# Kernel optimization log

Measured on AMD Instinct MI355X. Metric: run time of the kernel, lower is better.

Reference implementation:

```python
import jax, jax.numpy as jnp
import numpy as np

B, N, C, H, K = 4, 16384, 256, 8, 64
D = C // H
EPS = 1e-8

def setup_inputs() -> dict:
    key = jax.random.key(0)
    ks = jax.random.split(key, 6)
    scale = 0.02
    return {
        "voxel_features": jax.random.normal(ks[0], (B, N, C), dtype=jnp.float32),
        "cluster_assignments": jax.random.uniform(ks[1], (B, N, K), dtype=jnp.float32),
        "w_qkv": jax.random.normal(ks[2], (C, 3 * C), dtype=jnp.float32) * scale,
        "w_proj": jax.random.normal(ks[3], (C, C), dtype=jnp.float32) * scale,
        "b_proj": jnp.zeros((C,), dtype=jnp.float32),
        "cluster_bias": jax.random.normal(ks[4], (K, K), dtype=jnp.float32) * scale,
    }

def reference(voxel_features, cluster_assignments, w_qkv, w_proj, b_proj, cluster_bias):
    b, n, c = voxel_features.shape
    h, d = H, c // H
    A = cluster_assignments                                  # (B,N,K)
    qkv = (voxel_features @ w_qkv).reshape(b, n, 3, h, d)    # (B,N,3,H,D)
    q = jnp.moveaxis(qkv[:, :, 0], 1, 2)                     # (B,H,N,D)
    k = jnp.moveaxis(qkv[:, :, 1], 1, 2)
    v = jnp.moveaxis(qkv[:, :, 2], 1, 2)
    # cluster mass per (batch, cluster)
    denom = A.sum(axis=1) + EPS                              # (B,K)
    # cluster-pooled K/V: contraction over N (the huge broadcast-sum in torch)
    k_cluster = jnp.einsum('bnk,bhnd->bhkd', A, k) / denom[:, None, :, None]
    v_cluster = jnp.einsum('bnk,bhnd->bhkd', A, v) / denom[:, None, :, None]
    attn = jnp.einsum('bhnd,bhkd->bhnk', q, k_cluster) * (d ** -0.5)
    bias = jnp.einsum('bnk,kl->bnl', A, cluster_bias)        # (B,N,K)
    attn = jax.nn.softmax(attn + bias[:, None, :, :], axis=-1)
    x = jnp.einsum('bhnk,bhkd->bhnd', attn, v_cluster)       # (B,H,N,D)
    x = jnp.moveaxis(x, 1, 2).reshape(b, n, c)               # (B,N,C)
    return x @ w_proj + b_proj
```

## Files before the change

### kernel.cpp

```cpp
#include <hip/hip_runtime.h>

#define NTOK 16384
#define BATCH 4

typedef __attribute__((ext_vector_type(8))) short bf16x8;
typedef __attribute__((ext_vector_type(8))) unsigned short ushort8;
typedef __attribute__((ext_vector_type(4))) float f32x4;

__device__ __forceinline__ unsigned short f2bf(float f) {
  union { float f; unsigned int u; } c; c.f = f;
  unsigned int r = c.u + 0x7fff + ((c.u >> 16) & 1);
  return (unsigned short)(r >> 16);
}

__global__ __launch_bounds__(256) void zero_f(float* __restrict__ p, int n) {
  int i = blockIdx.x * 256 + threadIdx.x;
  if (i < n) p[i] = 0.f;
}

__global__ __launch_bounds__(256) void convx2(const float* __restrict__ voxel,
                                              const float* __restrict__ A,
                                              unsigned short* __restrict__ xb,
                                              unsigned short* __restrict__ Ab) {
  for (int i = blockIdx.x * 256 + threadIdx.x; i < 2621440; i += gridDim.x * 256) {
    const float* src; unsigned short* dst; int j;
    if (i < 2097152) { j = i; src = voxel; dst = xb; }
    else { j = i - 2097152; src = A; dst = Ab; }
    float4 a = *(const float4*)(src + 8 * (size_t)j);
    float4 b = *(const float4*)(src + 8 * (size_t)j + 4);
    ushort8 o;
    o[0] = f2bf(a.x); o[1] = f2bf(a.y); o[2] = f2bf(a.z); o[3] = f2bf(a.w);
    o[4] = f2bf(b.x); o[5] = f2bf(b.y); o[6] = f2bf(b.z); o[7] = f2bf(b.w);
    *(ushort8*)(dst + 8 * (size_t)j) = o;
  }
}

__global__ __launch_bounds__(256) void convw(const float* __restrict__ w_qkv,
                                             const float* __restrict__ w_proj,
                                             const float* __restrict__ cb,
                                             unsigned short* __restrict__ wqT,
                                             unsigned short* __restrict__ wpT,
                                             unsigned short* __restrict__ cbbT) {
  int n = blockIdx.x, k = threadIdx.x;
  if (n < 256) wqT[n * 256 + k] = f2bf(w_qkv[(size_t)k * 768 + n]);
  else if (n < 512) wpT[(n - 256) * 256 + k] = f2bf(w_proj[(size_t)k * 256 + (n - 256)]);
  else if (n == 512 && k < 64) {
    for (int j = 0; j < 64; ++j) cbbT[k * 64 + j] = f2bf(cb[j * 64 + k]);
  }
}

template <int ADD_BIAS, int C_BF16>
__global__ __launch_bounds__(256, 3) void gemm_mfma(const unsigned short* __restrict__ Ab,
                                                    const unsigned short* __restrict__ BT,
                                                    const float* __restrict__ bias,
                                                    void* __restrict__ Cv,
                                                    int N, int K, int lda) {
  __shared__ __align__(16) unsigned short smem[2][128][72];
  const int tid = threadIdx.x;
  int bx, by;
  if ((gridDim.y & 7) == 0) {
    int flat = blockIdx.y * gridDim.x + blockIdx.x;
    int xc = flat & 7, t = flat >> 3;
    int gx = gridDim.x, ypx = gridDim.y >> 3;
    bx = t % gx; by = xc * ypx + t / gx;
  } else { bx = blockIdx.x; by = blockIdx.y; }
  const int bn = bx * 128, bm = by * 128;
  const int lane = tid & 63;
  const int wv = tid >> 6;
  const int wm = wv & 1, wn = wv >> 1;
  const int m16 = lane & 15, quad = lane >> 4;

  const int srow = tid >> 1;
  const int scol = (tid & 1) * 32;

  const unsigned short* ga = Ab + (size_t)(bm + srow) * lda + scol;
  const unsigned short* gb = BT + (size_t)(bn + srow) * K + scol;

  ushort8 ra[2][4], rb[2][4];
#pragma unroll
  for (int kt = 0; kt < 2; ++kt)
#pragma unroll
    for (int i = 0; i < 4; ++i) {
      ra[kt][i] = *(const ushort8*)(ga + kt * 64 + 8 * i);
      rb[kt][i] = *(const ushort8*)(gb + kt * 64 + 8 * i);
    }

  f32x4 acc[4][4];
#pragma unroll
  for (int r = 0; r < 4; ++r)
#pragma unroll
    for (int c = 0; c < 4; ++c) acc[r][c] = (f32x4){0.f, 0.f, 0.f, 0.f};

#pragma unroll
  for (int kt = 0; kt < 4; ++kt) {
    const int sb = kt & 1;
    if (kt > 0) __syncthreads();
#pragma unroll
    for (int i = 0; i < 4; ++i) {
      *(ushort8*)&smem[0][srow][scol + 8 * i] = ra[sb][i];
      *(ushort8*)&smem[1][srow][scol + 8 * i] = rb[sb][i];
    }
    __syncthreads();
    if (kt < 2) {
#pragma unroll
      for (int i = 0; i < 4; ++i) {
        ra[sb][i] = *(const ushort8*)(ga + (kt + 2) * 64 + 8 * i);
        rb[sb][i] = *(const ushort8*)(gb + (kt + 2) * 64 + 8 * i);
      }
    }
#pragma unroll
    for (int ks = 0; ks < 64; ks += 32) {
      bf16x8 af[4], bf[4];
#pragma unroll
      for (int r = 0; r < 4; ++r)
        af[r] = *(const bf16x8*)&smem[0][wm * 64 + r * 16 + m16][ks + quad * 8];
#pragma unroll
      for (int c = 0; c < 4; ++c)
        bf[c] = *(const bf16x8*)&smem[1][wn * 64 + c * 16 + m16][ks + quad * 8];
#pragma unroll
      for (int r = 0; r < 4; ++r)
#pragma unroll
        for (int c = 0; c < 4; ++c)
          acc[r][c] = __builtin_amdgcn_mfma_f32_16x16x32_bf16(af[r], bf[c], acc[r][c], 0, 0, 0);
    }
  }

  float bv[4];
  if (ADD_BIAS) {
#pragma unroll
    for (int c = 0; c < 4; ++c) bv[c] = bias[bn + wn * 64 + c * 16 + m16];
  }
  const int lrD = tid >> 2, cch = (tid & 3) * 32;
  unsigned short* Csh = (unsigned short*)smem;
  float* Csf = (float*)smem;
#pragma unroll
  for (int p = 0; p < 2; ++p) {
    __syncthreads();
    if (wm == p) {
#pragma unroll
      for (int r = 0; r < 4; ++r) {
        int lr0 = r * 16 + quad * 4;
#pragma unroll
        for (int c = 0; c < 4; ++c) {
          int col = wn * 64 + c * 16 + m16;
#pragma unroll
          for (int i = 0; i < 4; ++i) {
            float v = acc[r][c][i] + (ADD_BIAS ? bv[c] : 0.f);
            if (C_BF16) Csh[(lr0 + i) * 136 + col] = f2bf(v);
            else Csf[(lr0 + i) * 132 + col] = v;
          }
        }
      }
    }
    __syncthreads();
    if (C_BF16) {
      unsigned short* gp = (unsigned short*)Cv + (size_t)(bm + p * 64 + lrD) * N + bn + cch;
      const unsigned short* sp = Csh + lrD * 136 + cch;
      ushort8 t0 = *(const ushort8*)(sp + 0);
      ushort8 t1 = *(const ushort8*)(sp + 8);
      ushort8 t2 = *(const ushort8*)(sp + 16);
      ushort8 t3 = *(const ushort8*)(sp + 24);
      *(ushort8*)(gp + 0) = t0;
      *(ushort8*)(gp + 8) = t1;
      *(ushort8*)(gp + 16) = t2;
      *(ushort8*)(gp + 24) = t3;
    } else {
      float* gp = (float*)Cv + (size_t)(bm + p * 64 + lrD) * N + bn + cch;
      const float* sp = Csf + lrD * 132 + cch;
      float4 t[8];
#pragma unroll
      for (int u = 0; u < 8; ++u) t[u] = *(const float4*)(sp + 4 * u);
#pragma unroll
      for (int u = 0; u < 8; ++u) *(float4*)(gp + 4 * u) = t[u];
    }
  }
}

__global__ __launch_bounds__(256) void pool_mfma(const unsigned short* __restrict__ Ab,
                                                 const unsigned short* __restrict__ xb,
                                                 float* __restrict__ part) {
  __shared__ unsigned short At[64][40];
  __shared__ unsigned short Xt[128][40];
  const int tid = threadIdx.x;
  const int tch = blockIdx.x, cblk = blockIdx.y, b = blockIdx.z;
  const int w = tid >> 6, lane = tid & 63;
  const int m16 = lane & 15, quad = lane >> 4;
  const size_t row0 = (size_t)b * NTOK + (size_t)tch * 256;
  const int cb0 = cblk * 128;
  const int tokL = tid & 31, gA = tid >> 5;

  f32x4 acc[4][2];
#pragma unroll
  for (int r = 0; r < 4; ++r)
#pragma unroll
    for (int c = 0; c < 2; ++c) acc[r][c] = (f32x4){0.f, 0.f, 0.f, 0.f};

  ushort8 px[2], pa;
  auto loadG = [&](int t0) {
#pragma unroll
    for (int u = 0; u < 2; ++u) {
      int idx = tid + u * 256;
      int tok = idx & 31, g = idx >> 5;
      px[u] = *(const ushort8*)(xb + (row0 + t0 + tok) * 256 + cb0 + g * 8);
    }
    pa = *(const ushort8*)(Ab + (row0 + t0 + tokL) * 64 + gA * 8);
  };
  loadG(0);

  for (int ks = 0; ks < 8; ++ks) {
    __syncthreads();
#pragma unroll
    for (int u = 0; u < 2; ++u) {
      int idx = tid + u * 256;
      int tok = idx & 31, g = idx >> 5;
#pragma unroll
      for (int i = 0; i < 8; ++i) Xt[g * 8 + i][tok] = (unsigned short)px[u][i];
    }
#pragma unroll
    for (int i = 0; i < 8; ++i) At[gA * 8 + i][tokL] = (unsigned short)pa[i];
    __syncthreads();
    if (ks + 1 < 8) loadG((ks + 1) * 32);
    bf16x8 af[4], bfr[2];
#pragma unroll
    for (int r = 0; r < 4; ++r) af[r] = *(const bf16x8*)&At[r * 16 + m16][quad * 8];
#pragma unroll
    for (int c = 0; c < 2; ++c) bfr[c] = *(const bf16x8*)&Xt[w * 32 + c * 16 + m16][quad * 8];
#pragma unroll
    for (int r = 0; r < 4; ++r)
#pragma unroll
      for (int c = 0; c < 2; ++c)
        acc[r][c] = __builtin_amdgcn_mfma_f32_16x16x32_bf16(af[r], bfr[c], acc[r][c], 0, 0, 0);
  }

  float* pp = part + ((size_t)(b * 64 + tch) * 64) * 256 + cb0;
#pragma unroll
  for (int r = 0; r < 4; ++r)
#pragma unroll
    for (int c = 0; c < 2; ++c)
#pragma unroll
      for (int i = 0; i < 4; ++i) {
        int cl = r * 16 + quad * 4 + i;
        int ch = w * 32 + c * 16 + m16;
        pp[(size_t)cl * 256 + ch] = acc[r][c][i];
      }
}

__global__ __launch_bounds__(256) void pool2(const float* __restrict__ part,
                                             const float* __restrict__ asum,
                                             float* __restrict__ pooledX) {
  int id = blockIdx.x * 256 + threadIdx.x;
  int c = id & 255, cl = (id >> 8) & 63, b = id >> 14;
  const float* pp = part + ((size_t)(b * 64) * 64 + cl) * 256 + c;
  float s = 0.f;
#pragma unroll 4
  for (int t = 0; t < 64; ++t) s += pp[(size_t)t * 16384];
  float denom = asum[b * 64 + cl] + 1e-8f;
  pooledX[(size_t)(b * 64 + cl) * 256 + c] = s / denom;
}

__global__ __launch_bounds__(256) void kvgemm(const float* __restrict__ pooledX,
                                              const float* __restrict__ w_qkv,
                                              unsigned short* __restrict__ kcb,
                                              unsigned short* __restrict__ vcbT) {
  __shared__ float px[256];
  const int bc = blockIdx.x;
  const int b = bc >> 6, cl = bc & 63;
  const int tid = threadIdx.x;
  px[tid] = pooledX[(size_t)bc * 256 + tid];
  __syncthreads();
  float accK = 0.f, accV = 0.f;
#pragma unroll 8
  for (int k = 0; k < 256; ++k) {
    float x = px[k];
    accK = fmaf(x, w_qkv[(size_t)k * 768 + 256 + tid], accK);
    accV = fmaf(x, w_qkv[(size_t)k * 768 + 512 + tid], accV);
  }
  int h = tid >> 5, d = tid & 31;
  kcb[(((size_t)b * 8 + h) * 64 + cl) * 32 + d] = f2bf(accK * 0.17677669529663687f);
  vcbT[(((size_t)b * 8 + h) * 32 + d) * 64 + cl] = f2bf(accV);
}

__global__ __launch_bounds__(256) void asum_kernel(const float* __restrict__ A,
                                                   float* __restrict__ asum) {
  __shared__ float red[4][64];
  const int ch = blockIdx.x, b = blockIdx.y;
  const int jq = threadIdx.x >> 6, k = threadIdx.x & 63;
  const size_t row0 = (size_t)b * NTOK + (size_t)ch * 256;
  const float* ap = A + (row0 + jq) * 64 + k;
  float s = 0.f;
#pragma unroll 4
  for (int j = 0; j < 64; ++j) s += ap[(size_t)j * 256];
  red[jq][k] = s;
  __syncthreads();
  if (threadIdx.x < 64) {
    float v = red[0][k] + red[1][k] + red[2][k] + red[3][k];
    atomicAdd(&asum[b * 64 + k], v);
  }
}

__global__ __launch_bounds__(256) void attn_mfma(const unsigned short* __restrict__ Ab,
                                                 unsigned short* __restrict__ qb,
                                                 const unsigned short* __restrict__ kcb,
                                                 const unsigned short* __restrict__ vcbT,
                                                 const unsigned short* __restrict__ cbbT) {
  __shared__ __align__(16) char lds[38400];
  unsigned short* PA  = (unsigned short*)lds;
  unsigned short* Qs  = (unsigned short*)(lds + 18432);
  unsigned short* KCs = (unsigned short*)(lds + 28672);
  unsigned short* VTs = (unsigned short*)(lds + 33792);
  unsigned short* CBs = (unsigned short*)(lds + 28672);

  const int tid = threadIdx.x;
  const int nb = blockIdx.x, hq = blockIdx.y, b = blockIdx.z;
  const int h0 = hq * 4;
  const int w = tid >> 6, lane = tid & 63;
  const int m16 = lane & 15, quad = lane >> 4;
  const size_t row0 = (size_t)b * NTOK + (size_t)nb * 128;

  const int r2 = tid >> 1, half = tid & 1;
  const int l4 = tid >> 2, s3 = tid & 3;
  const int d8 = tid >> 3, s7 = tid & 7;

  ushort8 rA[4], rcb[2];
  {
    const unsigned short* ap = Ab + (row0 + r2) * 64 + half * 32;
#pragma unroll
    for (int u = 0; u < 4; ++u) rA[u] = *(const ushort8*)(ap + 8 * u);
    const unsigned short* cp = cbbT + l4 * 64 + s3 * 16;
    rcb[0] = *(const ushort8*)cp;
    rcb[1] = *(const ushort8*)(cp + 8);
  }
  ushort8 rq[2][2], rkc[2], rvt[2];
  {
    const unsigned short* qp = qb + (row0 + r2) * 256 + h0 * 32 + half * 16;
    rq[0][0] = *(const ushort8*)qp;
    rq[0][1] = *(const ushort8*)(qp + 8);
    rkc[0] = *(const ushort8*)(kcb + (((size_t)b * 8 + h0) * 64 + l4) * 32 + s3 * 8);
    rvt[0] = *(const ushort8*)(vcbT + (((size_t)b * 8 + h0) * 32 + d8) * 64 + s7 * 8);
  }
#pragma unroll
  for (int u = 0; u < 4; ++u) *(ushort8*)&PA[r2 * 72 + half * 32 + 8 * u] = rA[u];
  *(ushort8*)&CBs[l4 * 72 + s3 * 16] = rcb[0];
  *(ushort8*)&CBs[l4 * 72 + s3 * 16 + 8] = rcb[1];
  __syncthreads();

  f32x4 bacc[2][4];
#pragma unroll
  for (int rt = 0; rt < 2; ++rt)
#pragma unroll
    for (int nt = 0; nt < 4; ++nt) bacc[rt][nt] = (f32x4){0.f, 0.f, 0.f, 0.f};
#pragma unroll
  for (int ks = 0; ks < 64; ks += 32) {
    bf16x8 af[2], bf[4];
#pragma unroll
    for (int rt = 0; rt < 2; ++rt)
      af[rt] = *(const bf16x8*)&PA[(w * 32 + rt * 16 + m16) * 72 + ks + quad * 8];
#pragma unroll
    for (int nt = 0; nt < 4; ++nt)
      bf[nt] = *(const bf16x8*)&CBs[(nt * 16 + m16) * 72 + ks + quad * 8];
#pragma unroll
    for (int rt = 0; rt < 2; ++rt)
#pragma unroll
      for (int nt = 0; nt < 4; ++nt)
        bacc[rt][nt] = __builtin_amdgcn_mfma_f32_16x16x32_bf16(af[rt], bf[nt], bacc[rt][nt], 0, 0, 0);
  }
  __syncthreads();

#pragma unroll
  for (int hh = 0; hh < 4; ++hh) {
    const int h = h0 + hh;
    const int cur = hh & 1;
    *(ushort8*)&Qs[r2 * 40 + half * 16] = rq[cur][0];
    *(ushort8*)&Qs[r2 * 40 + half * 16 + 8] = rq[cur][1];
    *(ushort8*)&KCs[l4 * 40 + s3 * 8] = rkc[cur];
    *(ushort8*)&VTs[d8 * 72 + s7 * 8] = rvt[cur];
    if (hh < 3) {
      const int h1 = h + 1;
      const unsigned short* qp = qb + (row0 + r2) * 256 + h1 * 32 + half * 16;
      rq[cur ^ 1][0] = *(const ushort8*)qp;
      rq[cur ^ 1][1] = *(const ushort8*)(qp + 8);
      rkc[cur ^ 1] = *(const ushort8*)(kcb + (((size_t)b * 8 + h1) * 64 + l4) * 32 + s3 * 8);
      rvt[cur ^ 1] = *(const ushort8*)(vcbT + (((size_t)b * 8 + h1) * 32 + d8) * 64 + s7 * 8);
    }
    __syncthreads();

    f32x4 acc[2][4];
#pragma unroll
    for (int rt = 0; rt < 2; ++rt)
#pragma unroll
      for (int nt = 0; nt < 4; ++nt) acc[rt][nt] = bacc[rt][nt];
    {
      bf16x8 af[2], bf[4];
#pragma unroll
      for (int rt = 0; rt < 2; ++rt)
        af[rt] = *(const bf16x8*)&Qs[(w * 32 + rt * 16 + m16) * 40 + quad * 8];
#pragma unroll
      for (int nt = 0; nt < 4; ++nt)
        bf[nt] = *(const bf16x8*)&KCs[(nt * 16 + m16) * 40 + quad * 8];
#pragma unroll
      for (int rt = 0; rt < 2; ++rt)
#pragma unroll
        for (int nt = 0; nt < 4; ++nt)
          acc[rt][nt] = __builtin_amdgcn_mfma_f32_16x16x32_bf16(af[rt], bf[nt], acc[rt][nt], 0, 0, 0);
    }

#pragma unroll
    for (int rt = 0; rt < 2; ++rt) {
      f32x4 mxv, sv;
#pragma unroll
      for (int i = 0; i < 4; ++i)
        mxv[i] = fmaxf(fmaxf(acc[rt][0][i], acc[rt][1][i]),
                       fmaxf(acc[rt][2][i], acc[rt][3][i]));
#pragma unroll
      for (int msk = 1; msk < 16; msk <<= 1)
#pragma unroll
        for (int i = 0; i < 4; ++i) mxv[i] = fmaxf(mxv[i], __shfl_xor(mxv[i], msk));
#pragma unroll
      for (int i = 0; i < 4; ++i) sv[i] = 0.f;
#pragma unroll
      for (int nt = 0; nt < 4; ++nt)
#pragma unroll
        for (int i = 0; i < 4; ++i) {
          float e = __expf(acc[rt][nt][i] - mxv[i]);
          acc[rt][nt][i] = e;
          sv[i] += e;
        }
#pragma unroll
      for (int msk = 1; msk < 16; msk <<= 1)
#pragma unroll
        for (int i = 0; i < 4; ++i) sv[i] += __shfl_xor(sv[i], msk);
#pragma unroll
      for (int i = 0; i < 4; ++i) sv[i] = 1.f / sv[i];
#pragma unroll
      for (int nt = 0; nt < 4; ++nt)
#pragma unroll
        for (int i = 0; i < 4; ++i)
          PA[(w * 32 + rt * 16 + quad * 4 + i) * 72 + nt * 16 + m16] =
              f2bf(acc[rt][nt][i] * sv[i]);
    }

    f32x4 acc2[2][2];
#pragma unroll
    for (int rt = 0; rt < 2; ++rt)
#pragma unroll
      for (int nt = 0; nt < 2; ++nt) acc2[rt][nt] = (f32x4){0.f, 0.f, 0.f, 0.f};
#pragma unroll
    for (int kch = 0; kch < 64; kch += 32) {
      bf16x8 af2[2], bf2[2];
#pragma unroll
      for (int rt = 0; rt < 2; ++rt)
        af2[rt] = *(const bf16x8*)&PA[(w * 32 + rt * 16 + m16) * 72 + kch + quad * 8];
#pragma unroll
      for (int nt = 0; nt < 2; ++nt)
        bf2[nt] = *(const bf16x8*)&VTs[(nt * 16 + m16) * 72 + kch + quad * 8];
#pragma unroll
      for (int rt = 0; rt < 2; ++rt)
#pragma unroll
        for (int nt = 0; nt < 2; ++nt)
          acc2[rt][nt] = __builtin_amdgcn_mfma_f32_16x16x32_bf16(af2[rt], bf2[nt], acc2[rt][nt], 0, 0, 0);
    }

#pragma unroll
    for (int rt = 0; rt < 2; ++rt)
#pragma unroll
      for (int nt = 0; nt < 2; ++nt)
#pragma unroll
        for (int i = 0; i < 4; ++i) {
          int tr = w * 32 + rt * 16 + quad * 4 + i;
          int d = nt * 16 + m16;
          qb[(row0 + tr) * 256 + h * 32 + d] = f2bf(acc2[rt][nt][i]);
        }
    __syncthreads();
  }
}

extern "C" void kernel_launch(void* const* d_in, const int* in_sizes, int n_in,
                              void* d_out, int out_size, void* d_ws, size_t ws_size,
                              hipStream_t stream) {
  const float* voxel  = (const float*)d_in[0];
  const float* A      = (const float*)d_in[1];
  const float* w_qkv  = (const float*)d_in[2];
  const float* w_proj = (const float*)d_in[3];
  const float* b_proj = (const float*)d_in[4];
  const float* cb     = (const float*)d_in[5];
  float* out = (float*)d_out;
  (void)in_sizes; (void)n_in; (void)out_size; (void)ws_size;

  char* wsb = (char*)d_ws;
  unsigned short* qb       = (unsigned short*)wsb;
  unsigned short* xb       = (unsigned short*)(wsb + 33554432);
  float* part              = (float*)(wsb + 67108864);
  float* asum              = (float*)(wsb + 83886080);
  float* pooledXf          = (float*)(wsb + 83887104);
  unsigned short* wqT      = (unsigned short*)(wsb + 84149248);
  unsigned short* wpT      = (unsigned short*)(wsb + 84280320);
  unsigned short* kcb      = (unsigned short*)(wsb + 84411392);
  unsigned short* vcbT     = (unsigned short*)(wsb + 84542464);
  unsigned short* cbbT     = (unsigned short*)(wsb + 84673536);
  unsigned short* Ab = (unsigned short*)d_out;

  zero_f<<<1, 256, 0, stream>>>(asum, 256);
  convw<<<513, 256, 0, stream>>>(w_qkv, w_proj, cb, wqT, wpT, cbbT);
  convx2<<<2048, 256, 0, stream>>>(voxel, A, xb, Ab);

  gemm_mfma<0, 1><<<dim3(2, 512), 256, 0, stream>>>(xb, wqT, nullptr, qb,
                                                    256, 256, 256);

  asum_kernel<<<dim3(64, BATCH), 256, 0, stream>>>(A, asum);
  pool_mfma<<<dim3(64, 2, BATCH), 256, 0, stream>>>(Ab, xb, part);
  pool2<<<256, 256, 0, stream>>>(part, asum, pooledXf);
  kvgemm<<<256, 256, 0, stream>>>(pooledXf, w_qkv, kcb, vcbT);

  attn_mfma<<<dim3(NTOK / 128, 2, BATCH), 256, 0, stream>>>(Ab, qb, kcb, vcbT, cbbT);

  gemm_mfma<1, 0><<<dim3(2, 512), 256, 0, stream>>>(qb, wpT, b_proj, out,
                                                    256, 256, 256);
}
```

Before: 274.8 us.

## Fuse pool2 with kvgemm, fold zeroing into convw, restructure attention with exp2

```diff
diff --git a/kernel.cpp b/kernel.cpp
--- a/kernel.cpp
+++ b/kernel.cpp
@@ -13,9 +13,10 @@
   return (unsigned short)(r >> 16);
 }
 
-__global__ __launch_bounds__(256) void zero_f(float* __restrict__ p, int n) {
-  int i = blockIdx.x * 256 + threadIdx.x;
-  if (i < n) p[i] = 0.f;
+__device__ __forceinline__ float exp2_fast(float x) {
+  float r;
+  asm("v_exp_f32 %0, %1" : "=v"(r) : "v"(x));
+  return r;
 }
 
 __global__ __launch_bounds__(256) void convx2(const float* __restrict__ voxel,
@@ -40,12 +41,17 @@
                                              const float* __restrict__ cb,
                                              unsigned short* __restrict__ wqT,
                                              unsigned short* __restrict__ wpT,
-                                             unsigned short* __restrict__ cbbT) {
+                                             unsigned short* __restrict__ cbbT,
+                                             float* __restrict__ asum) {
   int n = blockIdx.x, k = threadIdx.x;
   if (n < 256) wqT[n * 256 + k] = f2bf(w_qkv[(size_t)k * 768 + n]);
   else if (n < 512) wpT[(n - 256) * 256 + k] = f2bf(w_proj[(size_t)k * 256 + (n - 256)]);
-  else if (n == 512 && k < 64) {
-    for (int j = 0; j < 64; ++j) cbbT[k * 64 + j] = f2bf(cb[j * 64 + k]);
+  else {
+    asum[k] = 0.f;
+    if (k < 64) {
+      for (int j = 0; j < 64; ++j)
+        cbbT[k * 64 + j] = f2bf(cb[j * 64 + k] * 1.4426950408889634f);
+    }
   }
 }
 
@@ -245,38 +251,32 @@
       }
 }
 
-__global__ __launch_bounds__(256) void pool2(const float* __restrict__ part,
-                                             const float* __restrict__ asum,
-                                             float* __restrict__ pooledX) {
-  int id = blockIdx.x * 256 + threadIdx.x;
-  int c = id & 255, cl = (id >> 8) & 63, b = id >> 14;
+__global__ __launch_bounds__(256) void pool2kv(const float* __restrict__ part,
+                                               const float* __restrict__ asum,
+                                               const float* __restrict__ w_qkv,
+                                               unsigned short* __restrict__ kcb,
+                                               unsigned short* __restrict__ vcbT) {
+  __shared__ float px[256];
+  const int bc = blockIdx.x;
+  const int b = bc >> 6, cl = bc & 63;
+  const int c = threadIdx.x;
   const float* pp = part + ((size_t)(b * 64) * 64 + cl) * 256 + c;
   float s = 0.f;
 #pragma unroll 4
   for (int t = 0; t < 64; ++t) s += pp[(size_t)t * 16384];
   float denom = asum[b * 64 + cl] + 1e-8f;
-  pooledX[(size_t)(b * 64 + cl) * 256 + c] = s / denom;
-}
-
-__global__ __launch_bounds__(256) void kvgemm(const float* __restrict__ pooledX,
-                                              const float* __restrict__ w_qkv,
-                                              unsigned short* __restrict__ kcb,
-                                              unsigned short* __restrict__ vcbT) {
-  __shared__ float px[256];
-  const int bc = blockIdx.x;
-  const int b = bc >> 6, cl = bc & 63;
-  const int tid = threadIdx.x;
-  px[tid] = pooledX[(size_t)bc * 256 + tid];
+  px[c] = s / denom;
   __syncthreads();
   float accK = 0.f, accV = 0.f;
 #pragma unroll 8
   for (int k = 0; k < 256; ++k) {
     float x = px[k];
-    accK = fmaf(x, w_qkv[(size_t)k * 768 + 256 + tid], accK);
-    accV = fmaf(x, w_qkv[(size_t)k * 768 + 512 + tid], accV);
-  }
-  int h = tid >> 5, d = tid & 31;
-  kcb[(((size_t)b * 8 + h) * 64 + cl) * 32 + d] = f2bf(accK * 0.17677669529663687f);
+    accK = fmaf(x, w_qkv[(size_t)k * 768 + 256 + c], accK);
+    accV = fmaf(x, w_qkv[(size_t)k * 768 + 512 + c], accV);
+  }
+  int h = c >> 5, d = c & 31;
+  kcb[(((size_t)b * 8 + h) * 64 + cl) * 32 + d] =
+      f2bf(accK * (0.17677669529663687f * 1.4426950408889634f));
   vcbT[(((size_t)b * 8 + h) * 32 + d) * 64 + cl] = f2bf(accV);
 }
 
@@ -303,174 +303,98 @@
                                                  const unsigned short* __restrict__ kcb,
                                                  const unsigned short* __restrict__ vcbT,
                                                  const unsigned short* __restrict__ cbbT) {
-  __shared__ __align__(16) char lds[38400];
-  unsigned short* PA  = (unsigned short*)lds;
-  unsigned short* Qs  = (unsigned short*)(lds + 18432);
-  unsigned short* KCs = (unsigned short*)(lds + 28672);
-  unsigned short* VTs = (unsigned short*)(lds + 33792);
-  unsigned short* CBs = (unsigned short*)(lds + 28672);
+  __shared__ __align__(16) unsigned short PA[64 * 72];
 
   const int tid = threadIdx.x;
-  const int nb = blockIdx.x, hq = blockIdx.y, b = blockIdx.z;
-  const int h0 = hq * 4;
+  const int nb = blockIdx.x, b = blockIdx.z;
   const int w = tid >> 6, lane = tid & 63;
   const int m16 = lane & 15, quad = lane >> 4;
-  const size_t row0 = (size_t)b * NTOK + (size_t)nb * 128;
-
-  const int r2 = tid >> 1, half = tid & 1;
-  const int l4 = tid >> 2, s3 = tid & 3;
-  const int d8 = tid >> 3, s7 = tid & 7;
-
-  ushort8 rA[4], rcb[2];
-  {
-    const unsigned short* ap = Ab + (row0 + r2) * 64 + half * 32;
-#pragma unroll
-    for (int u = 0; u < 4; ++u) rA[u] = *(const ushort8*)(ap + 8 * u);
-    const unsigned short* cp = cbbT + l4 * 64 + s3 * 16;
-    rcb[0] = *(const ushort8*)cp;
-    rcb[1] = *(const ushort8*)(cp + 8);
-  }
-  ushort8 rq[2][2], rkc[2], rvt[2];
-  {
-    const unsigned short* qp = qb + (row0 + r2) * 256 + h0 * 32 + half * 16;
-    rq[0][0] = *(const ushort8*)qp;
-    rq[0][1] = *(const ushort8*)(qp + 8);
-    rkc[0] = *(const ushort8*)(kcb + (((size_t)b * 8 + h0) * 64 + l4) * 32 + s3 * 8);
-    rvt[0] = *(const ushort8*)(vcbT + (((size_t)b * 8 + h0) * 32 + d8) * 64 + s7 * 8);
-  }
-#pragma unroll
-  for (int u = 0; u < 4; ++u) *(ushort8*)&PA[r2 * 72 + half * 32 + 8 * u] = rA[u];
-  *(ushort8*)&CBs[l4 * 72 + s3 * 16] = rcb[0];
-  *(ushort8*)&CBs[l4 * 72 + s3 * 16 + 8] = rcb[1];
-  __syncthreads();
-
-  f32x4 bacc[2][4];
-#pragma unroll
-  for (int rt = 0; rt < 2; ++rt)
-#pragma unroll
-    for (int nt = 0; nt < 4; ++nt) bacc[rt][nt] = (f32x4){0.f, 0.f, 0.f, 0.f};
-#pragma unroll
-  for (int ks = 0; ks < 64; ks += 32) {
-    bf16x8 af[2], bf[4];
-#pragma unroll
-    for (int rt = 0; rt < 2; ++rt)
-      af[rt] = *(const bf16x8*)&PA[(w * 32 + rt * 16 + m16) * 72 + ks + quad * 8];
+  const size_t row0 = (size_t)b * NTOK + (size_t)nb * 64;
+  const int rA = w * 16 + m16;
+  const size_t bh8 = (size_t)b * 8;
+
+  f32x4 bacc[4];
+#pragma unroll
+  for (int nt = 0; nt < 4; ++nt) bacc[nt] = (f32x4){0.f, 0.f, 0.f, 0.f};
+#pragma unroll
+  for (int ks = 0; ks < 2; ++ks) {
+    bf16x8 aA = *(const bf16x8*)(Ab + (row0 + rA) * 64 + ks * 32 + quad * 8);
+#pragma unroll
+    for (int nt = 0; nt < 4; ++nt) {
+      bf16x8 cbf = *(const bf16x8*)(cbbT + (nt * 16 + m16) * 64 + ks * 32 + quad * 8);
+      bacc[nt] = __builtin_amdgcn_mfma_f32_16x16x32_bf16(aA, cbf, bacc[nt], 0, 0, 0);
+    }
+  }
+
+  for (int h = 0; h < 8; ++h) {
+    bf16x8 qf = *(const bf16x8*)(qb + (row0 + rA) * 256 + h * 32 + quad * 8);
+    bf16x8 kcf[4];
 #pragma unroll
     for (int nt = 0; nt < 4; ++nt)
-      bf[nt] = *(const bf16x8*)&CBs[(nt * 16 + m16) * 72 + ks + quad * 8];
-#pragma unroll
-    for (int rt = 0; rt < 2; ++rt)
-#pragma unroll
-      for (int nt = 0; nt < 4; ++nt)
-        bacc[rt][nt] = __builtin_amdgcn_mfma_f32_16x16x32_bf16(af[rt], bf[nt], bacc[rt][nt], 0, 0, 0);
-  }
-  __syncthreads();
-
-#pragma unroll
-  for (int hh = 0; hh < 4; ++hh) {
-    const int h = h0 + hh;
-    const int cur = hh & 1;
-    *(ushort8*)&Qs[r2 * 40 + half * 16] = rq[cur][0];
-    *(ushort8*)&Qs[r2 * 40 + half * 16 + 8] = rq[cur][1];
-    *(ushort8*)&KCs[l4 * 40 + s3 * 8] = rkc[cur];
-    *(ushort8*)&VTs[d8 * 72 + s7 * 8] = rvt[cur];
-    if (hh < 3) {
-      const int h1 = h + 1;
-      const unsigned short* qp = qb + (row0 + r2) * 256 + h1 * 32 + half * 16;
-      rq[cur ^ 1][0] = *(const ushort8*)qp;
-      rq[cur ^ 1][1] = *(const ushort8*)(qp + 8);
-      rkc[cur ^ 1] = *(const ushort8*)(kcb + (((size_t)b * 8 + h1) * 64 + l4) * 32 + s3 * 8);
-      rvt[cur ^ 1] = *(const ushort8*)(vcbT + (((size_t)b * 8 + h1) * 32 + d8) * 64 + s7 * 8);
-    }
-    __syncthreads();
-
-    f32x4 acc[2][4];
-#pragma unroll
-    for (int rt = 0; rt < 2; ++rt)
-#pragma unroll
-      for (int nt = 0; nt < 4; ++nt) acc[rt][nt] = bacc[rt][nt];
-    {
-      bf16x8 af[2], bf[4];
-#pragma unroll
-      for (int rt = 0; rt < 2; ++rt)
-        af[rt] = *(const bf16x8*)&Qs[(w * 32 + rt * 16 + m16) * 40 + quad * 8];
-#pragma unroll
-      for (int nt = 0; nt < 4; ++nt)
-        bf[nt] = *(const bf16x8*)&KCs[(nt * 16 + m16) * 40 + quad * 8];
-#pragma unroll
-      for (int rt = 0; rt < 2; ++rt)
-#pragma unroll
-        for (int nt = 0; nt < 4; ++nt)
-          acc[rt][nt] = __builtin_amdgcn_mfma_f32_16x16x32_bf16(af[rt], bf[nt], acc[rt][nt], 0, 0, 0);
-    }
-
-#pragma unroll
-    for (int rt = 0; rt < 2; ++rt) {
-      f32x4 mxv, sv;
+      kcf[nt] = *(const bf16x8*)(kcb + ((bh8 + h) * 64 + nt * 16 + m16) * 32 + quad * 8);
+    bf16x8 vtf[2][2];
+#pragma unroll
+    for (int nt2 = 0; nt2 < 2; ++nt2)
+#pragma unroll
+      for (int kc2 = 0; kc2 < 2; ++kc2)
+        vtf[nt2][kc2] = *(const bf16x8*)(vcbT + ((bh8 + h) * 32 + nt2 * 16 + m16) * 64 +
+                                         kc2 * 32 + quad * 8);
+
+    f32x4 acc[4];
+#pragma unroll
+    for (int nt = 0; nt < 4; ++nt) {
+      acc[nt] = bacc[nt];
+      acc[nt] = __builtin_amdgcn_mfma_f32_16x16x32_bf16(qf, kcf[nt], acc[nt], 0, 0, 0);
+    }
+
+    f32x4 mxv, sv;
+#pragma unroll
+    for (int i = 0; i < 4; ++i)
+      mxv[i] = fmaxf(fmaxf(acc[0][i], acc[1][i]), fmaxf(acc[2][i], acc[3][i]));
+#pragma unroll
+    for (int msk = 1; msk < 16; msk <<= 1)
+#pragma unroll
+      for (int i = 0; i < 4; ++i) mxv[i] = fmaxf(mxv[i], __shfl_xor(mxv[i], msk));
+#pragma unroll
+    for (int i = 0; i < 4; ++i) sv[i] = 0.f;
+#pragma unroll
+    for (int nt = 0; nt < 4; ++nt)
+#pragma unroll
+      for (int i = 0; i < 4; ++i) {
+        float e = exp2_fast(acc[nt][i] - mxv[i]);
+        acc[nt][i] = e;
+        sv[i] += e;
+      }
+#pragma unroll
+    for (int msk = 1; msk < 16; msk <<= 1)
+#pragma unroll
+      for (int i = 0; i < 4; ++i) sv[i] += __shfl_xor(sv[i], msk);
+#pragma unroll
+    for (int i = 0; i < 4; ++i) sv[i] = 1.f / sv[i];
+
+#pragma unroll
+    for (int nt = 0; nt < 4; ++nt)
 #pragma unroll
       for (int i = 0; i < 4; ++i)
-        mxv[i] = fmaxf(fmaxf(acc[rt][0][i], acc[rt][1][i]),
-                       fmaxf(acc[rt][2][i], acc[rt][3][i]));
-#pragma unroll
-      for (int msk = 1; msk < 16; msk <<= 1)
-#pragma unroll
-        for (int i = 0; i < 4; ++i) mxv[i] = fmaxf(mxv[i], __shfl_xor(mxv[i], msk));
-#pragma unroll
-      for (int i = 0; i < 4; ++i) sv[i] = 0.f;
-#pragma unroll
-      for (int nt = 0; nt < 4; ++nt)
-#pragma unroll
-        for (int i = 0; i < 4; ++i) {
-          float e = __expf(acc[rt][nt][i] - mxv[i]);
-          acc[rt][nt][i] = e;
-          sv[i] += e;
-        }
-#pragma unroll
-      for (int msk = 1; msk < 16; msk <<= 1)
-#pragma unroll
-        for (int i = 0; i < 4; ++i) sv[i] += __shfl_xor(sv[i], msk);
-#pragma unroll
-      for (int i = 0; i < 4; ++i) sv[i] = 1.f / sv[i];
-#pragma unroll
-      for (int nt = 0; nt < 4; ++nt)
-#pragma unroll
-        for (int i = 0; i < 4; ++i)
-          PA[(w * 32 + rt * 16 + quad * 4 + i) * 72 + nt * 16 + m16] =
-              f2bf(acc[rt][nt][i] * sv[i]);
-    }
-
-    f32x4 acc2[2][2];
-#pragma unroll
-    for (int rt = 0; rt < 2; ++rt)
-#pragma unroll
-      for (int nt = 0; nt < 2; ++nt) acc2[rt][nt] = (f32x4){0.f, 0.f, 0.f, 0.f};
-#pragma unroll
-    for (int kch = 0; kch < 64; kch += 32) {
-      bf16x8 af2[2], bf2[2];
-#pragma unroll
-      for (int rt = 0; rt < 2; ++rt)
-        af2[rt] = *(const bf16x8*)&PA[(w * 32 + rt * 16 + m16) * 72 + kch + quad * 8];
-#pragma unroll
-      for (int nt = 0; nt < 2; ++nt)
-        bf2[nt] = *(const bf16x8*)&VTs[(nt * 16 + m16) * 72 + kch + quad * 8];
-#pragma unroll
-      for (int rt = 0; rt < 2; ++rt)
-#pragma unroll
-        for (int nt = 0; nt < 2; ++nt)
-          acc2[rt][nt] = __builtin_amdgcn_mfma_f32_16x16x32_bf16(af2[rt], bf2[nt], acc2[rt][nt], 0, 0, 0);
-    }
-
-#pragma unroll
-    for (int rt = 0; rt < 2; ++rt)
-#pragma unroll
-      for (int nt = 0; nt < 2; ++nt)
-#pragma unroll
-        for (int i = 0; i < 4; ++i) {
-          int tr = w * 32 + rt * 16 + quad * 4 + i;
-          int d = nt * 16 + m16;
-          qb[(row0 + tr) * 256 + h * 32 + d] = f2bf(acc2[rt][nt][i]);
-        }
-    __syncthreads();
+        PA[(w * 16 + quad * 4 + i) * 72 + nt * 16 + m16] = f2bf(acc[nt][i] * sv[i]);
+
+    f32x4 acc2[2];
+#pragma unroll
+    for (int nt2 = 0; nt2 < 2; ++nt2) acc2[nt2] = (f32x4){0.f, 0.f, 0.f, 0.f};
+#pragma unroll
+    for (int kc2 = 0; kc2 < 2; ++kc2) {
+      bf16x8 pf = *(const bf16x8*)&PA[rA * 72 + kc2 * 32 + quad * 8];
+#pragma unroll
+      for (int nt2 = 0; nt2 < 2; ++nt2)
+        acc2[nt2] = __builtin_amdgcn_mfma_f32_16x16x32_bf16(pf, vtf[nt2][kc2], acc2[nt2], 0, 0, 0);
+    }
+
+#pragma unroll
+    for (int nt2 = 0; nt2 < 2; ++nt2)
+#pragma unroll
+      for (int i = 0; i < 4; ++i)
+        qb[(row0 + w * 16 + quad * 4 + i) * 256 + h * 32 + nt2 * 16 + m16] =
+            f2bf(acc2[nt2][i]);
   }
 }
 
@@ -491,7 +415,6 @@
   unsigned short* xb       = (unsigned short*)(wsb + 33554432);
   float* part              = (float*)(wsb + 67108864);
   float* asum              = (float*)(wsb + 83886080);
-  float* pooledXf          = (float*)(wsb + 83887104);
   unsigned short* wqT      = (unsigned short*)(wsb + 84149248);
   unsigned short* wpT      = (unsigned short*)(wsb + 84280320);
   unsigned short* kcb      = (unsigned short*)(wsb + 84411392);
@@ -499,8 +422,7 @@
   unsigned short* cbbT     = (unsigned short*)(wsb + 84673536);
   unsigned short* Ab = (unsigned short*)d_out;
 
-  zero_f<<<1, 256, 0, stream>>>(asum, 256);
-  convw<<<513, 256, 0, stream>>>(w_qkv, w_proj, cb, wqT, wpT, cbbT);
+  convw<<<513, 256, 0, stream>>>(w_qkv, w_proj, cb, wqT, wpT, cbbT, asum);
   convx2<<<2048, 256, 0, stream>>>(voxel, A, xb, Ab);
 
   gemm_mfma<0, 1><<<dim3(2, 512), 256, 0, stream>>>(xb, wqT, nullptr, qb,
@@ -508,10 +430,9 @@
 
   asum_kernel<<<dim3(64, BATCH), 256, 0, stream>>>(A, asum);
   pool_mfma<<<dim3(64, 2, BATCH), 256, 0, stream>>>(Ab, xb, part);
-  pool2<<<256, 256, 0, stream>>>(part, asum, pooledXf);
-  kvgemm<<<256, 256, 0, stream>>>(pooledXf, w_qkv, kcb, vcbT);
-
-  attn_mfma<<<dim3(NTOK / 128, 2, BATCH), 256, 0, stream>>>(Ab, qb, kcb, vcbT, cbbT);
+  pool2kv<<<256, 256, 0, stream>>>(part, asum, w_qkv, kcb, vcbT);
+
+  attn_mfma<<<dim3(NTOK / 64, 1, BATCH), 256, 0, stream>>>(Ab, qb, kcb, vcbT, cbbT);
 
   gemm_mfma<1, 0><<<dim3(2, 512), 256, 0, stream>>>(qb, wpT, b_proj, out,
                                                     256, 256, 256);
```

New measurement: 277.7 us. Within noise of the previous version (+1.1%).
